# Optimization experiments

Hardware: AMD Instinct MI355X
Metric: run time of the kernel (lower is better)

## Reference

```python
import jax, jax.numpy as jnp
import numpy as np

D_IN = 1024
D_OUT = 1024
SEQ = 4096


def setup_inputs() -> dict:
    key = jax.random.key(0)
    kx, kq, kk, kv = jax.random.split(key, 4)
    s = 1.0 / np.sqrt(D_IN)
    return {
        "x": jax.random.normal(kx, (SEQ, D_IN), dtype=jnp.float32),
        # nn.Linear weights: shape [d_out, d_in], applied as x @ W.T
        "W_q": jax.random.uniform(kq, (D_OUT, D_IN), dtype=jnp.float32, minval=-s, maxval=s),
        "W_k": jax.random.uniform(kk, (D_OUT, D_IN), dtype=jnp.float32, minval=-s, maxval=s),
        "W_v": jax.random.uniform(kv, (D_OUT, D_IN), dtype=jnp.float32, minval=-s, maxval=s),
    }


def reference(x, W_q, W_k, W_v):
    # QKV projections (no bias)
    q = x @ W_q.T  # [N, d_out]
    k = x @ W_k.T
    v = x @ W_v.T
    d_k = k.shape[-1]
    scores = (q @ k.T) / jnp.sqrt(jnp.asarray(d_k, x.dtype))  # [N, N]
    attn = jax.nn.softmax(scores, axis=1)
    n = attn.shape[0]
    mask = jnp.tril(jnp.ones((n, n), dtype=attn.dtype))
    causal = attn * mask
    causal = causal / jnp.sum(causal, axis=1, keepdims=True)
    return causal @ v  # [N, d_out]
```

## Files before the change

### kernel.cpp

```cpp
#include <hip/hip_runtime.h>
#include <hip/hip_bf16.h>
#include <stdint.h>
#include <math.h>

#define SEQ 4096
#define DIM 1024

typedef __attribute__((ext_vector_type(8))) __bf16 bf16x8;
typedef __attribute__((ext_vector_type(4))) float f32x4;
typedef __attribute__((ext_vector_type(8))) unsigned short u16x8;

__device__ __forceinline__ unsigned short f2bf(float f) {
  unsigned int u = __float_as_uint(f);
  u = (u + 0x7FFFu + ((u >> 16) & 1u)) >> 16;
  return (unsigned short)u;
}

__device__ __forceinline__ int swz(int o) { return o ^ (((o >> 7) & 7) << 4); }

template <int N> __device__ __forceinline__ void wait_vm() {
  if constexpr (N == 0) asm volatile("s_waitcnt vmcnt(0)" ::: "memory");
  else if constexpr (N == 6) asm volatile("s_waitcnt vmcnt(6)" ::: "memory");
  else if constexpr (N == 8) asm volatile("s_waitcnt vmcnt(8)" ::: "memory");
}

__global__ void __launch_bounds__(256) cvt_all(const float* __restrict__ x,
                                               const float* __restrict__ wq,
                                               const float* __restrict__ wk,
                                               const float* __restrict__ wv,
                                               unsigned short* __restrict__ xb,
                                               unsigned short* __restrict__ wqk,
                                               unsigned short* __restrict__ wvb) {
  const int bid = blockIdx.x;
  const float* src;
  unsigned short* dst;
  size_t base;
  if (bid < 2048)      { src = x;  dst = xb;                base = (size_t)bid * 2048; }
  else if (bid < 2560) { src = wq; dst = wqk;               base = (size_t)(bid - 2048) * 2048; }
  else if (bid < 3072) { src = wk; dst = wqk + 1024 * 1024; base = (size_t)(bid - 2560) * 2048; }
  else                 { src = wv; dst = wvb;               base = (size_t)(bid - 3072) * 2048; }
  size_t i = base + (size_t)threadIdx.x * 8;
  float4 a = *reinterpret_cast<const float4*>(src + i);
  float4 b = *reinterpret_cast<const float4*>(src + i + 4);
  u16x8 o;
  o[0] = f2bf(a.x); o[1] = f2bf(a.y); o[2] = f2bf(a.z); o[3] = f2bf(a.w);
  o[4] = f2bf(b.x); o[5] = f2bf(b.y); o[6] = f2bf(b.z); o[7] = f2bf(b.w);
  *reinterpret_cast<u16x8*>(dst + i) = o;
}

__device__ __forceinline__ void gemm128_64(const unsigned short* __restrict__ A,
                                           const unsigned short* __restrict__ B,
                                           unsigned short* __restrict__ C,
                                           unsigned short* As, unsigned short* Bs,
                                           int lda, int ldb, int ldc,
                                           int tr, int tc, float scale) {
  constexpr int NT = 16;
  const int tid = threadIdx.x;
  const int lane = tid & 63;
  const int wid = tid >> 6;
  const int wr = wid >> 1, wc = wid & 1;
  const int l15 = lane & 15;
  const int kq = lane >> 4;

  f32x4 acc[4][4];
  #pragma unroll
  for (int m = 0; m < 4; ++m)
    #pragma unroll
    for (int n = 0; n < 4; ++n)
      acc[m][n] = (f32x4){0.f, 0.f, 0.f, 0.f};

  const unsigned short* Abase = A + (size_t)tr * 128 * lda;
  const unsigned short* Bbase = B + (size_t)tc * 128 * ldb;

  auto stage = [&](int buf, int kt) {
    const int k0 = kt << 6;
    #pragma unroll
    for (int i = 0; i < 4; ++i) {
      const int o = (i * 256 + tid) * 16;
      const int cs = (swz(o) >> 4) & 7;
      const unsigned short* ga = Abase + (size_t)(o >> 7) * lda + k0 + cs * 8;
      const unsigned short* gb = Bbase + (size_t)(o >> 7) * ldb + k0 + cs * 8;
      __builtin_amdgcn_global_load_lds(
          (const __attribute__((address_space(1))) unsigned int*)ga,
          (__attribute__((address_space(3))) unsigned int*)((char*)(As + buf * 8192) + o), 16, 0, 0);
      __builtin_amdgcn_global_load_lds(
          (const __attribute__((address_space(1))) unsigned int*)gb,
          (__attribute__((address_space(3))) unsigned int*)((char*)(Bs + buf * 8192) + o), 16, 0, 0);
    }
  };

  stage(0, 0);
  int cur = 0;
  for (int kt = 0; kt < NT; ++kt) {
    if (kt + 1 < NT) { stage(cur ^ 1, kt + 1); wait_vm<8>(); }
    else wait_vm<0>();
    __builtin_amdgcn_s_barrier();

    bf16x8 af[4][2], bv[4][2];
    #pragma unroll
    for (int m = 0; m < 4; ++m)
      #pragma unroll
      for (int ks = 0; ks < 2; ++ks) {
        const int row = wr * 64 + m * 16 + l15;
        af[m][ks] = *reinterpret_cast<const bf16x8*>(
            (const char*)(As + cur * 8192) + swz(row * 128 + kq * 16 + ks * 64));
      }
    #pragma unroll
    for (int n = 0; n < 4; ++n)
      #pragma unroll
      for (int ks = 0; ks < 2; ++ks) {
        const int row = wc * 64 + n * 16 + l15;
        bv[n][ks] = *reinterpret_cast<const bf16x8*>(
            (const char*)(Bs + cur * 8192) + swz(row * 128 + kq * 16 + ks * 64));
      }
    __builtin_amdgcn_s_setprio(1);
    #pragma unroll
    for (int m = 0; m < 4; ++m)
      #pragma unroll
      for (int n = 0; n < 4; ++n) {
        acc[m][n] = __builtin_amdgcn_mfma_f32_16x16x32_bf16(af[m][0], bv[n][0], acc[m][n], 0, 0, 0);
        acc[m][n] = __builtin_amdgcn_mfma_f32_16x16x32_bf16(af[m][1], bv[n][1], acc[m][n], 0, 0, 0);
      }
    __builtin_amdgcn_s_setprio(0);
    __builtin_amdgcn_s_barrier();
    cur ^= 1;
  }

  const int rbase = tr * 128 + wr * 64 + kq * 4;
  const int cbase = tc * 128 + wc * 64 + l15;
  #pragma unroll
  for (int m = 0; m < 4; ++m)
    #pragma unroll
    for (int n = 0; n < 4; ++n)
      #pragma unroll
      for (int i = 0; i < 4; ++i)
        C[(size_t)(rbase + m * 16 + i) * ldc + cbase + n * 16] = f2bf(acc[m][n][i] * scale);
}

__global__ void __launch_bounds__(256) projvt_kernel(const unsigned short* __restrict__ xb,
                                                     const unsigned short* __restrict__ wqk,
                                                     const unsigned short* __restrict__ wvb,
                                                     unsigned short* __restrict__ qkb,
                                                     unsigned short* __restrict__ vt) {
  __shared__ __align__(16) unsigned short As[2 * 128 * 64];
  __shared__ __align__(16) unsigned short Bs[2 * 128 * 64];
  const int bid = (blockIdx.x & 7) * 96 + (blockIdx.x >> 3);
  if (bid < 512) {
    gemm128_64(xb, wqk, qkb, As, Bs, DIM, DIM, 2048, bid >> 4, bid & 15, 1.0f);
  } else {
    const int t = bid - 512;
    gemm128_64(wvb, xb, vt, As, Bs, DIM, DIM, SEQ, t >> 5, t & 31, 1.0f);
  }
}

__global__ void __launch_bounds__(256) qkt_kernel(const unsigned short* __restrict__ qkb,
                                                  unsigned short* __restrict__ S) {
  __shared__ __align__(16) unsigned short As[2 * 128 * 64];
  __shared__ __align__(16) unsigned short Bs[2 * 128 * 64];
  const int b = (blockIdx.x & 7) * 66 + (blockIdx.x >> 3);
  int tr = (int)((sqrtf(8.0f * b + 1.0f) - 1.0f) * 0.5f);
  while ((tr + 1) * (tr + 2) / 2 <= b) ++tr;
  while (tr * (tr + 1) / 2 > b) --tr;
  const int tc = b - tr * (tr + 1) / 2;
  gemm128_64(qkb, qkb + 1024, S, As, Bs, 2048, 2048, SEQ, tr, tc, 0.03125f);
}

__global__ void __launch_bounds__(256) pv_kernel(const unsigned short* __restrict__ A,
                                                 const unsigned short* __restrict__ B,
                                                 float* __restrict__ C,
                                                 float* __restrict__ P1, float* __restrict__ P2,
                                                 float* __restrict__ P3) {
  constexpr int BM = 64;
  constexpr int lda = SEQ, ldb = SEQ, ldc = DIM;
  int tc = blockIdx.x, tr = blockIdx.y;
  const int s = blockIdx.z;
  const int ltiles = tr + 1;
  int kt0 = s * 16;
  if (kt0 >= ltiles) return;
  const int nt = min(ltiles, kt0 + 16) - kt0;

  __shared__ __align__(16) unsigned short As[2][BM * 64];
  __shared__ __align__(16) unsigned short Bs[2][128 * 64];

  const int tid = threadIdx.x;
  const int lane = tid & 63;
  const int wid = tid >> 6;
  const int wr = wid >> 1, wc = wid & 1;
  const int l15 = lane & 15;
  const int kq = lane >> 4;

  f32x4 acc[2][4];
  #pragma unroll
  for (int m = 0; m < 2; ++m)
    #pragma unroll
    for (int n = 0; n < 4; ++n)
      acc[m][n] = (f32x4){0.f, 0.f, 0.f, 0.f};

  const unsigned short* Abase = A + (size_t)tr * BM * lda;
  const unsigned short* Bbase = B + (size_t)tc * 128 * ldb;

  auto stage = [&](int buf, int ktabs) {
    const int k0 = ktabs << 6;
    #pragma unroll
    for (int i = 0; i < 2; ++i) {
      const int o = (i * 256 + tid) * 16;
      const int cs = (swz(o) >> 4) & 7;
      const unsigned short* g = Abase + (size_t)(o >> 7) * lda + k0 + cs * 8;
      __builtin_amdgcn_global_load_lds(
          (const __attribute__((address_space(1))) unsigned int*)g,
          (__attribute__((address_space(3))) unsigned int*)((char*)&As[buf][0] + o), 16, 0, 0);
    }
    #pragma unroll
    for (int i = 0; i < 4; ++i) {
      const int o = (i * 256 + tid) * 16;
      const int cs = (swz(o) >> 4) & 7;
      const unsigned short* g = Bbase + (size_t)(o >> 7) * ldb + k0 + cs * 8;
      __builtin_amdgcn_global_load_lds(
          (const __attribute__((address_space(1))) unsigned int*)g,
          (__attribute__((address_space(3))) unsigned int*)((char*)&Bs[buf][0] + o), 16, 0, 0);
    }
  };

  stage(0, kt0);
  int cur = 0;
  for (int kt = 0; kt < nt; ++kt) {
    if (kt + 1 < nt) { stage(cur ^ 1, kt0 + kt + 1); wait_vm<6>(); }
    else wait_vm<0>();
    __builtin_amdgcn_s_barrier();

    bf16x8 af[2][2], bv[4][2];
    #pragma unroll
    for (int m = 0; m < 2; ++m)
      #pragma unroll
      for (int ks = 0; ks < 2; ++ks) {
        const int row = wr * 32 + m * 16 + l15;
        af[m][ks] = *reinterpret_cast<const bf16x8*>(
            (const char*)&As[cur][0] + swz(row * 128 + kq * 16 + ks * 64));
      }
    #pragma unroll
    for (int n = 0; n < 4; ++n)
      #pragma unroll
      for (int ks = 0; ks < 2; ++ks) {
        const int row = wc * 64 + n * 16 + l15;
        bv[n][ks] = *reinterpret_cast<const bf16x8*>(
            (const char*)&Bs[cur][0] + swz(row * 128 + kq * 16 + ks * 64));
      }
    #pragma unroll
    for (int m = 0; m < 2; ++m)
      #pragma unroll
      for (int n = 0; n < 4; ++n) {
        acc[m][n] = __builtin_amdgcn_mfma_f32_16x16x32_bf16(af[m][0], bv[n][0], acc[m][n], 0, 0, 0);
        acc[m][n] = __builtin_amdgcn_mfma_f32_16x16x32_bf16(af[m][1], bv[n][1], acc[m][n], 0, 0, 0);
      }
    __builtin_amdgcn_s_barrier();
    cur ^= 1;
  }

  float* fdst = C;
  int rowoff = 0;
  if (s == 1) { fdst = P1; rowoff = 1024; }
  else if (s == 2) { fdst = P2; rowoff = 2048; }
  else if (s == 3) { fdst = P3; rowoff = 3072; }
  const int rbase = tr * BM + wr * 32 + kq * 4;
  const int cbase = tc * 128 + wc * 64 + l15;
  #pragma unroll
  for (int m = 0; m < 2; ++m)
    #pragma unroll
    for (int n = 0; n < 4; ++n)
      #pragma unroll
      for (int i = 0; i < 4; ++i)
        fdst[(size_t)(rbase + m * 16 + i - rowoff) * ldc + cbase + n * 16] = acc[m][n][i];
}

__global__ void __launch_bounds__(256) reduce_kernel(float* __restrict__ out,
                                                     const float* __restrict__ p1,
                                                     const float* __restrict__ p2,
                                                     const float* __restrict__ p3) {
  const int b = blockIdx.x;
  const size_t e = ((size_t)b * 1024) + threadIdx.x * 4;
  f32x4 acc = *reinterpret_cast<f32x4*>(out + (size_t)1024 * 1024 + e);
  acc += *reinterpret_cast<const f32x4*>(p1 + e);
  if (b >= 1024) acc += *reinterpret_cast<const f32x4*>(p2 + e - (size_t)1024 * 1024);
  if (b >= 2048) acc += *reinterpret_cast<const f32x4*>(p3 + e - (size_t)2048 * 1024);
  *reinterpret_cast<f32x4*>(out + (size_t)1024 * 1024 + e) = acc;
}

__global__ void __launch_bounds__(256) softmax_causal(unsigned short* __restrict__ S) {
  const int row = blockIdx.x;
  const int limit = ((row >> 6) + 1) << 6;
  unsigned short* Srow = S + (size_t)row * SEQ;
  const int tid = threadIdx.x;
  const int lane = tid & 63, wid = tid >> 6;

  float vals[16];
  bool act[2];
  #pragma unroll
  for (int i = 0; i < 2; ++i) {
    const int j0 = (tid + i * 256) * 8;
    act[i] = j0 < limit;
    if (act[i]) {
      const uint4 w = *reinterpret_cast<const uint4*>(Srow + j0);
      const unsigned int wb[4] = {w.x, w.y, w.z, w.w};
      #pragma unroll
      for (int e = 0; e < 4; ++e) {
        vals[i * 8 + 2 * e]     = __uint_as_float(wb[e] << 16);
        vals[i * 8 + 2 * e + 1] = __uint_as_float(wb[e] & 0xFFFF0000u);
      }
    } else {
      #pragma unroll
      for (int e = 0; e < 8; ++e) vals[i * 8 + e] = -1e30f;
    }
  }

  float m = -1e30f;
  #pragma unroll
  for (int i = 0; i < 2; ++i)
    #pragma unroll
    for (int e = 0; e < 8; ++e) {
      int j = (tid + i * 256) * 8 + e;
      if (j <= row) m = fmaxf(m, vals[i * 8 + e]);
    }
  #pragma unroll
  for (int off = 32; off > 0; off >>= 1) m = fmaxf(m, __shfl_xor(m, off));
  __shared__ float redm[4], reds[4];
  if (lane == 0) redm[wid] = m;
  __syncthreads();
  m = fmaxf(fmaxf(redm[0], redm[1]), fmaxf(redm[2], redm[3]));

  float s = 0.f;
  float ev[16];
  #pragma unroll
  for (int i = 0; i < 2; ++i)
    #pragma unroll
    for (int e = 0; e < 8; ++e) {
      int j = (tid + i * 256) * 8 + e;
      float ex = (j <= row) ? __expf(vals[i * 8 + e] - m) : 0.f;
      ev[i * 8 + e] = ex;
      s += ex;
    }
  #pragma unroll
  for (int off = 32; off > 0; off >>= 1) s += __shfl_xor(s, off);
  if (lane == 0) reds[wid] = s;
  __syncthreads();
  s = reds[0] + reds[1] + reds[2] + reds[3];
  const float inv = 1.f / s;

  #pragma unroll
  for (int i = 0; i < 2; ++i) {
    if (!act[i]) continue;
    u16x8 o;
    #pragma unroll
    for (int e = 0; e < 8; ++e) o[e] = f2bf(ev[i * 8 + e] * inv);
    *reinterpret_cast<u16x8*>(Srow + (tid + i * 256) * 8) = o;
  }
}

extern "C" void kernel_launch(void* const* d_in, const int* in_sizes, int n_in,
                              void* d_out, int out_size, void* d_ws, size_t ws_size,
                              hipStream_t stream) {
  const float* x  = (const float*)d_in[0];
  const float* Wq = (const float*)d_in[1];
  const float* Wk = (const float*)d_in[2];
  const float* Wv = (const float*)d_in[3];
  float* out = (float*)d_out;

  char* ws = (char*)d_ws;
  const size_t MB = 1u << 20;
  unsigned short* xb   = (unsigned short*)(ws + 0 * MB);
  unsigned short* wqk  = (unsigned short*)(ws + 8 * MB);
  unsigned short* wvb  = (unsigned short*)(ws + 12 * MB);
  unsigned short* qkb  = (unsigned short*)(ws + 14 * MB);
  unsigned short* vt   = (unsigned short*)(ws + 30 * MB);
  unsigned short* S    = (unsigned short*)(ws + 38 * MB);
  float* p1 = (float*)(ws + 0 * MB);
  float* p2 = (float*)(ws + 12 * MB);
  float* p3 = (float*)(ws + 20 * MB);

  cvt_all<<<3584, 256, 0, stream>>>(x, Wq, Wk, Wv, xb, wqk, wvb);

  projvt_kernel<<<768, 256, 0, stream>>>(xb, wqk, wvb, qkb, vt);

  qkt_kernel<<<528, 256, 0, stream>>>(qkb, S);

  softmax_causal<<<SEQ, 256, 0, stream>>>(S);

  pv_kernel<<<dim3(DIM / 128, SEQ / 64, 4), 256, 0, stream>>>(S, vt, out, p1, p2, p3);
  reduce_kernel<<<3072, 256, 0, stream>>>(out, p1, p2, p3);
}
```

Measured before the change: 141.3 us.

## Split QK and V projections, pair softmax rows, drop swizzles and setprio

Splits the fused QK/V-transpose projection launch into two kernels, with a new 512-thread V^T GEMM kernel that has 8 waves each computing a 32x64 subtile. Softmax now handles two rows per 512-thread block, pairing a short causal row with a long one to balance the work. It also removes the XCD-aware block-index remapping in the projection and QK^T kernels and the s_setprio calls around the MFMA loop. These changes aim to improve occupancy and load balance, but they add an extra launch and may lose L2 locality on each XCD.

```diff
diff --git a/kernel.cpp b/kernel.cpp
--- a/kernel.cpp
+++ b/kernel.cpp
@@ -20,6 +20,7 @@
 
 template <int N> __device__ __forceinline__ void wait_vm() {
   if constexpr (N == 0) asm volatile("s_waitcnt vmcnt(0)" ::: "memory");
+  else if constexpr (N == 4) asm volatile("s_waitcnt vmcnt(4)" ::: "memory");
   else if constexpr (N == 6) asm volatile("s_waitcnt vmcnt(6)" ::: "memory");
   else if constexpr (N == 8) asm volatile("s_waitcnt vmcnt(8)" ::: "memory");
 }
@@ -113,7 +114,6 @@
         bv[n][ks] = *reinterpret_cast<const bf16x8*>(
             (const char*)(Bs + cur * 8192) + swz(row * 128 + kq * 16 + ks * 64));
       }
-    __builtin_amdgcn_s_setprio(1);
     #pragma unroll
     for (int m = 0; m < 4; ++m)
       #pragma unroll
@@ -121,7 +121,6 @@
         acc[m][n] = __builtin_amdgcn_mfma_f32_16x16x32_bf16(af[m][0], bv[n][0], acc[m][n], 0, 0, 0);
         acc[m][n] = __builtin_amdgcn_mfma_f32_16x16x32_bf16(af[m][1], bv[n][1], acc[m][n], 0, 0, 0);
       }
-    __builtin_amdgcn_s_setprio(0);
     __builtin_amdgcn_s_barrier();
     cur ^= 1;
   }
@@ -137,27 +136,107 @@
         C[(size_t)(rbase + m * 16 + i) * ldc + cbase + n * 16] = f2bf(acc[m][n][i] * scale);
 }
 
-__global__ void __launch_bounds__(256) projvt_kernel(const unsigned short* __restrict__ xb,
-                                                     const unsigned short* __restrict__ wqk,
-                                                     const unsigned short* __restrict__ wvb,
-                                                     unsigned short* __restrict__ qkb,
-                                                     unsigned short* __restrict__ vt) {
+__global__ void __launch_bounds__(256) proj_qk(const unsigned short* __restrict__ xb,
+                                               const unsigned short* __restrict__ wqk,
+                                               unsigned short* __restrict__ qkb) {
   __shared__ __align__(16) unsigned short As[2 * 128 * 64];
   __shared__ __align__(16) unsigned short Bs[2 * 128 * 64];
-  const int bid = (blockIdx.x & 7) * 96 + (blockIdx.x >> 3);
-  if (bid < 512) {
-    gemm128_64(xb, wqk, qkb, As, Bs, DIM, DIM, 2048, bid >> 4, bid & 15, 1.0f);
-  } else {
-    const int t = bid - 512;
-    gemm128_64(wvb, xb, vt, As, Bs, DIM, DIM, SEQ, t >> 5, t & 31, 1.0f);
+  gemm128_64(xb, wqk, qkb, As, Bs, DIM, DIM, 2048, blockIdx.x >> 4, blockIdx.x & 15, 1.0f);
+}
+
+__global__ void __launch_bounds__(512) vt_kernel(const unsigned short* __restrict__ wvb,
+                                                 const unsigned short* __restrict__ xb,
+                                                 unsigned short* __restrict__ vt) {
+  __shared__ __align__(16) unsigned short A0[2 * 128 * 64];
+  __shared__ __align__(16) unsigned short B0[2 * 128 * 64];
+  const int tid = threadIdx.x;
+  const int lane = tid & 63;
+  const int wid = tid >> 6;
+  const int wr = wid >> 1;
+  const int wc = wid & 1;
+  const int l15 = lane & 15;
+  const int kq = lane >> 4;
+
+  const int t = blockIdx.x;
+  const int tr = t >> 5, tc = t & 31;
+  const unsigned short* Abase = wvb + (size_t)tr * 128 * DIM;
+  const unsigned short* Bbase = xb + (size_t)tc * 128 * DIM;
+
+  f32x4 acc[2][4];
+  #pragma unroll
+  for (int m = 0; m < 2; ++m)
+    #pragma unroll
+    for (int n = 0; n < 4; ++n)
+      acc[m][n] = (f32x4){0.f, 0.f, 0.f, 0.f};
+
+  auto stage = [&](int buf, int kt) {
+    const int k0 = kt << 6;
+    #pragma unroll
+    for (int i = 0; i < 2; ++i) {
+      const int o = (i * 512 + tid) * 16;
+      const int cs = (swz(o) >> 4) & 7;
+      const unsigned short* ga = Abase + (size_t)(o >> 7) * DIM + k0 + cs * 8;
+      const unsigned short* gb = Bbase + (size_t)(o >> 7) * DIM + k0 + cs * 8;
+      __builtin_amdgcn_global_load_lds(
+          (const __attribute__((address_space(1))) unsigned int*)ga,
+          (__attribute__((address_space(3))) unsigned int*)((char*)(A0 + buf * 128 * 64) + o), 16, 0, 0);
+      __builtin_amdgcn_global_load_lds(
+          (const __attribute__((address_space(1))) unsigned int*)gb,
+          (__attribute__((address_space(3))) unsigned int*)((char*)(B0 + buf * 128 * 64) + o), 16, 0, 0);
+    }
+  };
+
+  stage(0, 0);
+  int cur = 0;
+  for (int kt = 0; kt < 16; ++kt) {
+    if (kt + 1 < 16) { stage(cur ^ 1, kt + 1); wait_vm<4>(); }
+    else wait_vm<0>();
+    __builtin_amdgcn_s_barrier();
+
+    bf16x8 af[2][2], bv[4][2];
+    #pragma unroll
+    for (int m = 0; m < 2; ++m)
+      #pragma unroll
+      for (int ks = 0; ks < 2; ++ks) {
+        const int row = wr * 32 + m * 16 + l15;
+        af[m][ks] = *reinterpret_cast<const bf16x8*>(
+            (const char*)(A0 + cur * 128 * 64) + swz(row * 128 + kq * 16 + ks * 64));
+      }
+    #pragma unroll
+    for (int n = 0; n < 4; ++n)
+      #pragma unroll
+      for (int ks = 0; ks < 2; ++ks) {
+        const int row = wc * 64 + n * 16 + l15;
+        bv[n][ks] = *reinterpret_cast<const bf16x8*>(
+            (const char*)(B0 + cur * 128 * 64) + swz(row * 128 + kq * 16 + ks * 64));
+      }
+    #pragma unroll
+    for (int m = 0; m < 2; ++m)
+      #pragma unroll
+      for (int n = 0; n < 4; ++n) {
+        acc[m][n] = __builtin_amdgcn_mfma_f32_16x16x32_bf16(af[m][0], bv[n][0], acc[m][n], 0, 0, 0);
+        acc[m][n] = __builtin_amdgcn_mfma_f32_16x16x32_bf16(af[m][1], bv[n][1], acc[m][n], 0, 0, 0);
+      }
+    __builtin_amdgcn_s_barrier();
+    cur ^= 1;
   }
+
+  const int rbase = tr * 128 + wr * 32 + kq * 4;
+  const int cbase = tc * 128 + wc * 64 + l15;
+  #pragma unroll
+  for (int m = 0; m < 2; ++m)
+    #pragma unroll
+    for (int n = 0; n < 4; ++n)
+      #pragma unroll
+      for (int i = 0; i < 4; ++i)
+        vt[(size_t)(rbase + m * 16 + i) * SEQ + cbase + n * 16] = f2bf(acc[m][n][i]);
 }
 
 __global__ void __launch_bounds__(256) qkt_kernel(const unsigned short* __restrict__ qkb,
                                                   unsigned short* __restrict__ S) {
   __shared__ __align__(16) unsigned short As[2 * 128 * 64];
   __shared__ __align__(16) unsigned short Bs[2 * 128 * 64];
-  const int b = (blockIdx.x & 7) * 66 + (blockIdx.x >> 3);
+  const int b = blockIdx.x;
   int tr = (int)((sqrtf(8.0f * b + 1.0f) - 1.0f) * 0.5f);
   while ((tr + 1) * (tr + 2) / 2 <= b) ++tr;
   while (tr * (tr + 1) / 2 > b) --tr;
@@ -285,12 +364,14 @@
   *reinterpret_cast<f32x4*>(out + (size_t)1024 * 1024 + e) = acc;
 }
 
-__global__ void __launch_bounds__(256) softmax_causal(unsigned short* __restrict__ S) {
-  const int row = blockIdx.x;
+__global__ void __launch_bounds__(512) softmax_causal2(unsigned short* __restrict__ S) {
+  const int g = threadIdx.x >> 8;
+  const int row = g ? (SEQ - 1 - blockIdx.x) : blockIdx.x;
+  const int tid = threadIdx.x & 255;
+  const int lane = threadIdx.x & 63;
+  const int wid = (threadIdx.x >> 6) & 3;
   const int limit = ((row >> 6) + 1) << 6;
   unsigned short* Srow = S + (size_t)row * SEQ;
-  const int tid = threadIdx.x;
-  const int lane = tid & 63, wid = tid >> 6;
 
   float vals[16];
   bool act[2];
@@ -322,10 +403,10 @@
     }
   #pragma unroll
   for (int off = 32; off > 0; off >>= 1) m = fmaxf(m, __shfl_xor(m, off));
-  __shared__ float redm[4], reds[4];
-  if (lane == 0) redm[wid] = m;
+  __shared__ float redm[2][4], reds[2][4];
+  if (lane == 0) redm[g][wid] = m;
   __syncthreads();
-  m = fmaxf(fmaxf(redm[0], redm[1]), fmaxf(redm[2], redm[3]));
+  m = fmaxf(fmaxf(redm[g][0], redm[g][1]), fmaxf(redm[g][2], redm[g][3]));
 
   float s = 0.f;
   float ev[16];
@@ -340,9 +421,9 @@
     }
   #pragma unroll
   for (int off = 32; off > 0; off >>= 1) s += __shfl_xor(s, off);
-  if (lane == 0) reds[wid] = s;
+  if (lane == 0) reds[g][wid] = s;
   __syncthreads();
-  s = reds[0] + reds[1] + reds[2] + reds[3];
+  s = reds[g][0] + reds[g][1] + reds[g][2] + reds[g][3];
   const float inv = 1.f / s;
 
   #pragma unroll
@@ -378,11 +459,13 @@
 
   cvt_all<<<3584, 256, 0, stream>>>(x, Wq, Wk, Wv, xb, wqk, wvb);
 
-  projvt_kernel<<<768, 256, 0, stream>>>(xb, wqk, wvb, qkb, vt);
+  proj_qk<<<512, 256, 0, stream>>>(xb, wqk, qkb);
+
+  vt_kernel<<<256, 512, 0, stream>>>(wvb, xb, vt);
 
   qkt_kernel<<<528, 256, 0, stream>>>(qkb, S);
 
-  softmax_causal<<<SEQ, 256, 0, stream>>>(S);
+  softmax_causal2<<<SEQ / 2, 512, 0, stream>>>(S);
 
   pv_kernel<<<dim3(DIM / 128, SEQ / 64, 4), 256, 0, stream>>>(S, vt, out, p1, p2, p3);
   reduce_kernel<<<3072, 256, 0, stream>>>(out, p1, p2, p3);
```

Result: no change. 141.6 us (+0.2%).
